# Kernel tuning notes

Measured on AMD Instinct MI355X. Metric: run time of the kernel, lower is better.

## Reference

```python
import jax, jax.numpy as jnp
import numpy as np

D_MODEL = 1024
NUM_HEADS = 16
D_K = D_MODEL // NUM_HEADS
THETA = 10000.0


def setup_inputs() -> dict:
    key = jax.random.key(0)
    ks = jax.random.split(key, 5)
    B, S = 2, 2048
    sigma = np.sqrt(2.0 / (D_MODEL + D_MODEL))
    x = jax.random.normal(ks[0], (B, S, D_MODEL), dtype=jnp.float32)
    Wq = jax.random.normal(ks[1], (D_MODEL, D_MODEL), dtype=jnp.float32) * sigma
    Wk = jax.random.normal(ks[2], (D_MODEL, D_MODEL), dtype=jnp.float32) * sigma
    Wv = jax.random.normal(ks[3], (D_MODEL, D_MODEL), dtype=jnp.float32) * sigma
    Wo = jax.random.normal(ks[4], (D_MODEL, D_MODEL), dtype=jnp.float32) * sigma
    return {"x": x, "Wq": Wq, "Wk": Wk, "Wv": Wv, "Wo": Wo}


def _rope(x, cos, sin):
    # x: [B, H, S, D_K]; cos/sin: [S, D_K//2] broadcast to [1, 1, S, D_K//2]
    x1 = x[..., ::2]
    x2 = x[..., 1::2]
    even = x1 * cos - x2 * sin
    odd = x1 * sin + x2 * cos
    return jnp.stack((even, odd), axis=-1).reshape(x.shape)


def reference(x, Wq, Wk, Wv, Wo):
    B, S, _ = x.shape
    # projections: weight is (out, in), applied as einsum('oi,...i->...o')
    q = jnp.einsum('oi,bsi->bso', Wq, x).reshape(B, S, NUM_HEADS, D_K).transpose(0, 2, 1, 3)
    k = jnp.einsum('oi,bsi->bso', Wk, x).reshape(B, S, NUM_HEADS, D_K).transpose(0, 2, 1, 3)
    v = jnp.einsum('oi,bsi->bso', Wv, x).reshape(B, S, NUM_HEADS, D_K).transpose(0, 2, 1, 3)
    # RoPE tables (token_positions = arange(S))
    inv_freq = 1.0 / (THETA ** (jnp.arange(0, D_K, 2, dtype=jnp.float32) / D_K))
    t = jnp.arange(S, dtype=jnp.float32)
    freqs = t[:, None] * inv_freq[None, :]          # [S, D_K/2]
    cos = jnp.cos(freqs)[None, None]                # [1,1,S,D_K/2]
    sin = jnp.sin(freqs)[None, None]
    q = _rope(q, cos, sin)
    k = _rope(k, cos, sin)
    # causal attention, full materialized scores (faithful to source)
    scores = jnp.einsum('bhid,bhjd->bhij', q, k) / np.sqrt(D_K).astype(np.float32)
    causal = jnp.tril(jnp.ones((S, S), dtype=bool))
    scores = jnp.where(causal, scores, -jnp.inf)
    attn = jax.nn.softmax(scores, axis=-1)
    out = jnp.einsum('bhij,bhjd->bhid', attn, v)    # [B,H,S,D_K]
    out = out.transpose(0, 2, 1, 3).reshape(B, S, D_MODEL)
    return jnp.einsum('oi,bsi->bso', Wo, out)
```

## Files before the change

### kernel.cpp

```cpp
#include <hip/hip_runtime.h>

#define D_MODEL 1024
#define NUM_HEADS 16
#define SEQ 2048
#define BATCH 2

typedef __attribute__((ext_vector_type(8))) short bf16x8;
typedef __attribute__((ext_vector_type(4))) float f32x4;

__device__ __forceinline__ float bf2f(unsigned short u) {
    return __uint_as_float(((unsigned int)u) << 16);
}
__device__ __forceinline__ unsigned short f2bf(float f) {
    unsigned int u = __float_as_uint(f);
    return (unsigned short)((u + 0x7FFFu + ((u >> 16) & 1u)) >> 16);
}
__device__ __forceinline__ ushort4 pack4(float4 v) {
    return make_ushort4(f2bf(v.x), f2bf(v.y), f2bf(v.z), f2bf(v.w));
}

__device__ __forceinline__ void gload_lds16(const unsigned short* g, unsigned short* l) {
    __builtin_amdgcn_global_load_lds(
        (const __attribute__((address_space(1))) unsigned int*)g,
        (__attribute__((address_space(3))) unsigned int*)l,
        16, 0, 0);
}

__device__ __forceinline__ bf16x8 lds_read_swz(const unsigned short (*tile)[64], int row, int chunk) {
    const char* p = reinterpret_cast<const char*>(tile);
    return *reinterpret_cast<const bf16x8*>(p + row * 128 + (((chunk ^ (row & 7))) << 4));
}

__device__ __forceinline__ bf16x8 lds_read_swz32(const unsigned short (*tile)[32], int row, int chunk) {
    const char* p = reinterpret_cast<const char*>(tile);
    return *reinterpret_cast<const bf16x8*>(p + row * 64 + (((chunk ^ (row & 3))) << 4));
}

__device__ __forceinline__ bf16x8 lds_read_swz128(const unsigned short (*tile)[128], int row, int chunk) {
    const char* p = reinterpret_cast<const char*>(tile);
    return *reinterpret_cast<const bf16x8*>(p + row * 256 + (((chunk ^ (row & 15))) << 4));
}

__global__ __launch_bounds__(256) void conv_kernel(
    const float* __restrict__ src, unsigned short* __restrict__ dst, int n4)
{
    int i = blockIdx.x * 256 + threadIdx.x;
    if (i < n4) {
        float4 v = reinterpret_cast<const float4*>(src)[i];
        reinterpret_cast<ushort4*>(dst)[i] = pack4(v);
    }
}

__global__ __launch_bounds__(256) void conv4_kernel(
    const float* __restrict__ x, const float* __restrict__ Wq,
    const float* __restrict__ Wk, const float* __restrict__ Wv,
    unsigned short* __restrict__ xb, unsigned short* __restrict__ w3bf,
    float2* __restrict__ tab)
{
    int i = blockIdx.x * 256 + threadIdx.x;
    if (i < 1835008) {
        const float* src;
        unsigned short* dst;
        int off;
        if (i < 1048576) {
            src = x; dst = xb; off = i;
        } else {
            int j = i - 1048576;
            int which = j >> 18;
            off = j & 0x3FFFF;
            src = (which == 0) ? Wq : (which == 1) ? Wk : Wv;
            dst = w3bf + ((size_t)which << 20);
        }
        float4 v = reinterpret_cast<const float4*>(src)[off];
        reinterpret_cast<ushort4*>(dst)[off] = pack4(v);
    } else {
        int idx = i - 1835008;
        int s = idx >> 5, d2 = idx & 31;
        float inv = powf(10000.0f, -(float)d2 / 32.0f);
        float sn, cs;
        sincosf((float)s * inv, &sn, &cs);
        tab[idx] = make_float2(cs, sn);
    }
}

__global__ __launch_bounds__(256) void qkv_mfma_kernel(
    const unsigned short* __restrict__ xb,
    const unsigned short* __restrict__ w3,
    const float2* __restrict__ tab,
    unsigned short* __restrict__ qb, unsigned short* __restrict__ kb,
    unsigned short* __restrict__ vt)
{
    const int lin = blockIdx.x;
    const int b = lin & 7;
    const int t = lin >> 3;
    const int which = t % 3;
    const int y = t / 3;
    const unsigned short* __restrict__ W = w3 + (size_t)which * 1048576;
    const int m0 = y * 128;
    const int n0g = b * 128;

    __shared__ __align__(16) unsigned short As[2][128][32];
    __shared__ __align__(16) unsigned short Bs[2][128][32];

    const int tid = threadIdx.x;
    const int w = tid >> 6;
    const int lane = tid & 63;
    const int quad = lane >> 4;
    const int c15 = lane & 15;
    const int qm = w >> 1, qn = w & 1;
    const int srow4 = lane >> 2;
    const int sch4 = lane & 3;

    auto stage = [&](int k0, int buf) {
#pragma unroll
        for (int i = 0; i < 2; i++) {
            const int row = i * 64 + w * 16 + srow4;
            const int ch = sch4 ^ (row & 3);
            gload_lds16(xb + (size_t)(m0 + row) * 1024 + k0 + ch * 8,
                        &As[buf][i * 64 + w * 16][0]);
            gload_lds16(W + (size_t)(n0g + row) * 1024 + k0 + ch * 8,
                        &Bs[buf][i * 64 + w * 16][0]);
        }
    };

    f32x4 acc[4][4];
#pragma unroll
    for (int mi = 0; mi < 4; mi++)
#pragma unroll
        for (int ni = 0; ni < 4; ni++) acc[mi][ni] = (f32x4){0.f, 0.f, 0.f, 0.f};

    stage(0, 0);
    for (int k0 = 0; k0 < 1024; k0 += 32) {
        const int cb = (k0 >> 5) & 1;
        __syncthreads();
        if (k0 < 992) stage(k0 + 32, cb ^ 1);

        bf16x8 af[4], bfr[4];
#pragma unroll
        for (int mi = 0; mi < 4; mi++)
            af[mi] = lds_read_swz32(As[cb], qm * 64 + mi * 16 + c15, quad);
#pragma unroll
        for (int ni = 0; ni < 4; ni++)
            bfr[ni] = lds_read_swz32(Bs[cb], qn * 64 + ni * 16 + c15, quad);
#pragma unroll
        for (int mi = 0; mi < 4; mi++)
#pragma unroll
            for (int ni = 0; ni < 4; ni++)
                acc[mi][ni] = __builtin_amdgcn_mfma_f32_16x16x32_bf16(af[mi], bfr[ni], acc[mi][ni], 0, 0, 0);
    }

    __syncthreads();
    unsigned short* stg = &As[0][0][0] + w * (16 * 72);
    const int hq = b * 2 + qn;
    unsigned short* outp = (which == 0) ? qb : kb;
    const int odd = c15 & 1;

#pragma unroll
    for (int mi = 0; mi < 4; mi++) {
#pragma unroll
        for (int r = 0; r < 4; r++) {
            int m = m0 + qm * 64 + mi * 16 + quad * 4 + r;
            int s = m & (SEQ - 1);
            const float2* trow = tab + (s << 5);
#pragma unroll
            for (int ni = 0; ni < 4; ni++) {
                float val = acc[mi][ni][r];
                float res;
                if (which < 2) {
                    float part = __shfl_xor(val, 1);
                    float2 cs = trow[(ni * 16 + c15) >> 1];
                    res = odd ? (part * cs.y + val * cs.x) : (val * cs.x - part * cs.y);
                } else {
                    res = val;
                }
                stg[(quad * 4 + r) * 72 + ni * 16 + c15] = f2bf(res);
            }
        }
        if (which < 2) {
            int row = lane >> 2;
            int ch = lane & 3;
            int m = m0 + qm * 64 + mi * 16 + row;
            int s = m & (SEQ - 1);
            int bb = m >> 11;
            size_t ob = (((size_t)bb * NUM_HEADS + hq) * SEQ + s) * 64 + ch * 16;
            uint4 v0 = *reinterpret_cast<const uint4*>(&stg[row * 72 + ch * 16]);
            uint4 v1 = *reinterpret_cast<const uint4*>(&stg[row * 72 + ch * 16 + 8]);
            *reinterpret_cast<uint4*>(&outp[ob]) = v0;
            *reinterpret_cast<uint4*>(&outp[ob + 8]) = v1;
        } else {
            int mbase = m0 + qm * 64 + mi * 16;
            int bb = mbase >> 11;
            int s_base = mbase & (SEQ - 1);
            unsigned short tmp[16];
#pragma unroll
            for (int sl = 0; sl < 16; sl++) tmp[sl] = stg[sl * 72 + lane];
            size_t ob = (((size_t)bb * NUM_HEADS + hq) * 64 + lane) * SEQ + s_base;
            *reinterpret_cast<uint4*>(&vt[ob])     = *reinterpret_cast<uint4*>(&tmp[0]);
            *reinterpret_cast<uint4*>(&vt[ob + 8]) = *reinterpret_cast<uint4*>(&tmp[8]);
        }
    }
}

__global__ __launch_bounds__(256) void attn_kernel(
    const unsigned short* __restrict__ qb, const unsigned short* __restrict__ kb,
    const unsigned short* __restrict__ vt, unsigned short* __restrict__ ab)
{
    const int xpair = blockIdx.x;
    const int bh = blockIdx.y;
    const int b = bh >> 4, h = bh & 15;
    const size_t base = (size_t)bh * SEQ * 64;
    const size_t vbase = (size_t)bh * 64 * SEQ;
    const int tid = threadIdx.x;
    const int w = tid >> 6;
    const int lane = tid & 63;
    const int quad = lane >> 4;
    const int c15 = lane & 15;
    const int srow8 = lane >> 3;
    const int sch = lane & 7;
    const int srow16 = lane >> 4;
    const int sch16 = lane & 15;
    const float C = 0.125f;

    __shared__ __align__(16) unsigned short Ks[2][128][64];
    __shared__ __align__(16) unsigned short Vs[2][64][128];
    __shared__ __align__(16) unsigned short Pl[64][72];

    auto stage = [&](int sj, int buf) {
        const int j0s = sj * 128;
#pragma unroll
        for (int i = 0; i < 4; i++) {
            const int krow = w * 32 + i * 8 + srow8;
            const int kch = sch ^ (krow & 7);
            gload_lds16(kb + base + (size_t)(j0s + krow) * 64 + kch * 8,
                        &Ks[buf][w * 32 + i * 8][0]);
            const int vrow = w * 16 + i * 4 + srow16;
            const int vch = sch16 ^ (vrow & 15);
            gload_lds16(vt + vbase + (size_t)vrow * SEQ + j0s + vch * 8,
                        &Vs[buf][w * 16 + i * 4][0]);
        }
    };

    for (int pass = 0; pass < 2; pass++) {
        const int it = pass ? xpair : (31 - xpair);
        const int i0 = it * 64;
        const int nj = (it >> 1) + 1;

        const int qrow = i0 + w * 16 + c15;
        bf16x8 qf0 = *reinterpret_cast<const bf16x8*>(&qb[base + (size_t)qrow * 64 + quad * 8]);
        bf16x8 qf1 = *reinterpret_cast<const bf16x8*>(&qb[base + (size_t)qrow * 64 + 32 + quad * 8]);

        float m_st = -1e30f, l_st = 0.f;
        f32x4 Oc[4];
#pragma unroll
        for (int t = 0; t < 4; t++) Oc[t] = (f32x4){0.f, 0.f, 0.f, 0.f};

        __syncthreads();
        stage(0, 0);

        for (int sj = 0; sj < nj; sj++) {
            const int cb = sj & 1;

            __syncthreads();
            if (sj < nj - 1) stage(sj + 1, cb ^ 1);

#pragma unroll
            for (int hf = 0; hf < 2; hf++) {
                const int j0 = sj * 128 + hf * 64;
                if (j0 > i0) continue;

                bf16x8 kc0[4], kc1[4];
#pragma unroll
                for (int t = 0; t < 4; t++) {
                    kc0[t] = lds_read_swz(Ks[cb], hf * 64 + t * 16 + c15, quad);
                    kc1[t] = lds_read_swz(Ks[cb], hf * 64 + t * 16 + c15, 4 + quad);
                }

                f32x4 sc[4];
#pragma unroll
                for (int t = 0; t < 4; t++) sc[t] = (f32x4){0.f, 0.f, 0.f, 0.f};
                __builtin_amdgcn_s_setprio(1);
#pragma unroll
                for (int t = 0; t < 4; t++) {
                    sc[t] = __builtin_amdgcn_mfma_f32_16x16x32_bf16(kc0[t], qf0, sc[t], 0, 0, 0);
                    sc[t] = __builtin_amdgcn_mfma_f32_16x16x32_bf16(kc1[t], qf1, sc[t], 0, 0, 0);
                }
                __builtin_amdgcn_s_setprio(0);

                bf16x8 vv0[4], vv1[4];
#pragma unroll
                for (int t = 0; t < 4; t++) {
                    vv0[t] = lds_read_swz128(Vs[cb], t * 16 + c15, hf * 8 + quad);
                    vv1[t] = lds_read_swz128(Vs[cb], t * 16 + c15, hf * 8 + 4 + quad);
                }

                if (j0 == i0) {
                    const int gi = i0 + w * 16 + c15;
#pragma unroll
                    for (int t = 0; t < 4; t++) {
#pragma unroll
                        for (int r = 0; r < 4; r++) {
                            int gj = j0 + t * 16 + quad * 4 + r;
                            if (gj > gi) sc[t][r] = -1e30f;
                        }
                    }
                }

                float x0 = fmaxf(fmaxf(sc[0][0], sc[0][1]), fmaxf(sc[0][2], sc[0][3]));
                float x1 = fmaxf(fmaxf(sc[1][0], sc[1][1]), fmaxf(sc[1][2], sc[1][3]));
                float x2 = fmaxf(fmaxf(sc[2][0], sc[2][1]), fmaxf(sc[2][2], sc[2][3]));
                float x3 = fmaxf(fmaxf(sc[3][0], sc[3][1]), fmaxf(sc[3][2], sc[3][3]));
                float tm = fmaxf(fmaxf(x0, x1), fmaxf(x2, x3));
                tm = fmaxf(tm, __shfl_xor(tm, 16));
                tm = fmaxf(tm, __shfl_xor(tm, 32));

                if (!__all(tm <= m_st + 64.0f)) {
                    float mnew = fmaxf(m_st, tm);
                    float alpha = __expf((m_st - mnew) * C);
                    l_st *= alpha;
#pragma unroll
                    for (int t = 0; t < 4; t++)
#pragma unroll
                        for (int r = 0; r < 4; r++) Oc[t][r] *= alpha;
                    m_st = mnew;
                }

                const float mC = m_st * C;
                float p[4][4];
#pragma unroll
                for (int t = 0; t < 4; t++)
#pragma unroll
                    for (int r = 0; r < 4; r++)
                        p[t][r] = __expf(__builtin_fmaf(sc[t][r], C, -mC));

                float s0 = (p[0][0] + p[0][1]) + (p[0][2] + p[0][3]);
                float s1 = (p[1][0] + p[1][1]) + (p[1][2] + p[1][3]);
                float s2 = (p[2][0] + p[2][1]) + (p[2][2] + p[2][3]);
                float s3 = (p[3][0] + p[3][1]) + (p[3][2] + p[3][3]);
                l_st += (s0 + s1) + (s2 + s3);

#pragma unroll
                for (int t = 0; t < 4; t++) {
#pragma unroll
                    for (int hh = 0; hh < 2; hh++) {
                        unsigned int pk = (unsigned int)f2bf(p[t][2 * hh])
                                        | ((unsigned int)f2bf(p[t][2 * hh + 1]) << 16);
                        *reinterpret_cast<unsigned int*>(
                            &Pl[w * 16 + c15][t * 16 + quad * 4 + 2 * hh]) = pk;
                    }
                }

                bf16x8 ap0 = *reinterpret_cast<const bf16x8*>(&Pl[w * 16 + c15][quad * 8]);
                bf16x8 ap1 = *reinterpret_cast<const bf16x8*>(&Pl[w * 16 + c15][32 + quad * 8]);
                __builtin_amdgcn_s_setprio(1);
#pragma unroll
                for (int t = 0; t < 4; t++) {
                    Oc[t] = __builtin_amdgcn_mfma_f32_16x16x32_bf16(vv0[t], ap0, Oc[t], 0, 0, 0);
                    Oc[t] = __builtin_amdgcn_mfma_f32_16x16x32_bf16(vv1[t], ap1, Oc[t], 0, 0, 0);
                }
                __builtin_amdgcn_s_setprio(0);
            }
        }

        l_st += __shfl_xor(l_st, 16);
        l_st += __shfl_xor(l_st, 32);
        float inv = 1.0f / l_st;
#pragma unroll
        for (int t = 0; t < 4; t++) {
#pragma unroll
            for (int hh = 0; hh < 2; hh++) {
                unsigned int pk = (unsigned int)f2bf(Oc[t][2 * hh] * inv)
                                | ((unsigned int)f2bf(Oc[t][2 * hh + 1] * inv) << 16);
                *reinterpret_cast<unsigned int*>(
                    &Pl[w * 16 + c15][t * 16 + quad * 4 + 2 * hh]) = pk;
            }
        }
        {
            int row = lane >> 2;
            int ch = lane & 3;
            int gi = i0 + w * 16 + row;
            size_t ob = ((size_t)b * SEQ + gi) * 1024 + h * 64 + ch * 16;
            uint4 v0 = *reinterpret_cast<const uint4*>(&Pl[w * 16 + row][ch * 16]);
            uint4 v1 = *reinterpret_cast<const uint4*>(&Pl[w * 16 + row][ch * 16 + 8]);
            *reinterpret_cast<uint4*>(&ab[ob]) = v0;
            *reinterpret_cast<uint4*>(&ab[ob + 8]) = v1;
        }
    }
}

__global__ __launch_bounds__(256) void out_mfma_kernel(
    const unsigned short* __restrict__ A, const unsigned short* __restrict__ Wob,
    float* __restrict__ out)
{
    const int lin = blockIdx.x;
    const int b = lin & 7;
    const int y = lin >> 3;
    const int m0 = y * 64;
    const int n0g = b * 128;

    __shared__ __align__(16) unsigned short As[2][64][32];
    __shared__ __align__(16) unsigned short Bs[2][128][32];

    const int tid = threadIdx.x;
    const int w = tid >> 6;
    const int lane = tid & 63;
    const int quad = lane >> 4;
    const int c15 = lane & 15;
    const int qm = w >> 1, qn = w & 1;
    const int srow4 = lane >> 2;
    const int sch4 = lane & 3;

    auto stage = [&](int k0, int buf) {
        {
            const int row = w * 16 + srow4;
            const int ch = sch4 ^ (row & 3);
            gload_lds16(A + (size_t)(m0 + row) * 1024 + k0 + ch * 8,
                        &As[buf][w * 16][0]);
        }
#pragma unroll
        for (int i = 0; i < 2; i++) {
            const int row = i * 64 + w * 16 + srow4;
            const int ch = sch4 ^ (row & 3);
            gload_lds16(Wob + (size_t)(n0g + row) * 1024 + k0 + ch * 8,
                        &Bs[buf][i * 64 + w * 16][0]);
        }
    };

    f32x4 acc[2][4];
#pragma unroll
    for (int mi = 0; mi < 2; mi++)
#pragma unroll
        for (int ni = 0; ni < 4; ni++) acc[mi][ni] = (f32x4){0.f, 0.f, 0.f, 0.f};

    stage(0, 0);
    for (int k0 = 0; k0 < 1024; k0 += 32) {
        const int cb = (k0 >> 5) & 1;
        __syncthreads();
        if (k0 < 992) stage(k0 + 32, cb ^ 1);

        bf16x8 af[2], bfr[4];
#pragma unroll
        for (int mi = 0; mi < 2; mi++)
            af[mi] = lds_read_swz32(As[cb], qm * 32 + mi * 16 + c15, quad);
#pragma unroll
        for (int ni = 0; ni < 4; ni++)
            bfr[ni] = lds_read_swz32(Bs[cb], qn * 64 + ni * 16 + c15, quad);
#pragma unroll
        for (int mi = 0; mi < 2; mi++)
#pragma unroll
            for (int ni = 0; ni < 4; ni++)
                acc[mi][ni] = __builtin_amdgcn_mfma_f32_16x16x32_bf16(af[mi], bfr[ni], acc[mi][ni], 0, 0, 0);
    }

#pragma unroll
    for (int mi = 0; mi < 2; mi++) {
#pragma unroll
        for (int r = 0; r < 4; r++) {
            int m = m0 + qm * 32 + mi * 16 + quad * 4 + r;
#pragma unroll
            for (int ni = 0; ni < 4; ni++) {
                int n = n0g + qn * 64 + ni * 16 + c15;
                out[(size_t)m * 1024 + n] = acc[mi][ni][r];
            }
        }
    }
}

extern "C" void kernel_launch(void* const* d_in, const int* in_sizes, int n_in,
                              void* d_out, int out_size, void* d_ws, size_t ws_size,
                              hipStream_t stream)
{
    const float* x  = (const float*)d_in[0];
    const float* Wq = (const float*)d_in[1];
    const float* Wk = (const float*)d_in[2];
    const float* Wv = (const float*)d_in[3];
    const float* Wo = (const float*)d_in[4];
    float* out = (float*)d_out;

    const size_t QKV_ELEMS = (size_t)BATCH * SEQ * D_MODEL;

    unsigned short* qb = (unsigned short*)d_ws;
    unsigned short* kb = qb + QKV_ELEMS;
    unsigned short* vt = kb + QKV_ELEMS;
    unsigned short* ab = vt + QKV_ELEMS;
    unsigned short* w3bf = ab;
    unsigned short* wobf = qb;
    unsigned short* xbuf = (unsigned short*)d_out;
    float2* tab = (float2*)((char*)d_out + 8 * 1024 * 1024);

    conv4_kernel<<<dim3(7424), 256, 0, stream>>>(x, Wq, Wk, Wv, xbuf, w3bf, tab);
    qkv_mfma_kernel<<<dim3(768), 256, 0, stream>>>(xbuf, w3bf, tab, qb, kb, vt);
    attn_kernel<<<dim3(16, 32), 256, 0, stream>>>(qb, kb, vt, ab);
    conv_kernel<<<dim3(1024), 256, 0, stream>>>(Wo, wobf, 262144);
    out_mfma_kernel<<<dim3(512), 256, 0, stream>>>(ab, wobf, out);
}
```

Measured before the change: 202.3 us.

## Split attention KV tile across two wave groups with merged softmax states

Doubles the attention block to 512 threads so two groups of four waves each process one 64-column half of every 128-key tile in parallel, then merges their online-softmax states (max, sum, partial O) through shared memory at the end. The P matrix is now packed with v_cvt_pk_bf16_f32 and redistributed via cross-lane shuffles instead of a round trip through LDS. Staging work per thread is halved. This aims for more in-flight waves and shorter per-wave serial chains, at the cost of extra synchronisation and an end-of-tile reduction that reuses the K/V LDS buffers.

```diff
diff --git a/kernel.cpp b/kernel.cpp
--- a/kernel.cpp
+++ b/kernel.cpp
@@ -201,7 +201,7 @@
     }
 }
 
-__global__ __launch_bounds__(256) void attn_kernel(
+__global__ __launch_bounds__(512, 4) void attn_kernel(
     const unsigned short* __restrict__ qb, const unsigned short* __restrict__ kb,
     const unsigned short* __restrict__ vt, unsigned short* __restrict__ ab)
 {
@@ -212,6 +212,8 @@
     const size_t vbase = (size_t)bh * 64 * SEQ;
     const int tid = threadIdx.x;
     const int w = tid >> 6;
+    const int grp = w >> 2;
+    const int wa = w & 3;
     const int lane = tid & 63;
     const int quad = lane >> 4;
     const int c15 = lane & 15;
@@ -223,20 +225,22 @@
 
     __shared__ __align__(16) unsigned short Ks[2][128][64];
     __shared__ __align__(16) unsigned short Vs[2][64][128];
-    __shared__ __align__(16) unsigned short Pl[64][72];
+    float* exch = (float*)&Ks[0][0][0];
+    float2* ml  = (float2*)((char*)&Ks[0][0][0] + 17152);
+    unsigned short* ost = &Vs[0][0][0];
 
     auto stage = [&](int sj, int buf) {
         const int j0s = sj * 128;
 #pragma unroll
-        for (int i = 0; i < 4; i++) {
-            const int krow = w * 32 + i * 8 + srow8;
+        for (int i = 0; i < 2; i++) {
+            const int krow = w * 16 + i * 8 + srow8;
             const int kch = sch ^ (krow & 7);
             gload_lds16(kb + base + (size_t)(j0s + krow) * 64 + kch * 8,
-                        &Ks[buf][w * 32 + i * 8][0]);
-            const int vrow = w * 16 + i * 4 + srow16;
+                        &Ks[buf][w * 16 + i * 8][0]);
+            const int vrow = w * 8 + i * 4 + srow16;
             const int vch = sch16 ^ (vrow & 15);
             gload_lds16(vt + vbase + (size_t)vrow * SEQ + j0s + vch * 8,
-                        &Vs[buf][w * 16 + i * 4][0]);
+                        &Vs[buf][w * 8 + i * 4][0]);
         }
     };
 
@@ -245,7 +249,7 @@
         const int i0 = it * 64;
         const int nj = (it >> 1) + 1;
 
-        const int qrow = i0 + w * 16 + c15;
+        const int qrow = i0 + wa * 16 + c15;
         bf16x8 qf0 = *reinterpret_cast<const bf16x8*>(&qb[base + (size_t)qrow * 64 + quad * 8]);
         bf16x8 qf1 = *reinterpret_cast<const bf16x8*>(&qb[base + (size_t)qrow * 64 + 32 + quad * 8]);
 
@@ -259,20 +263,16 @@
 
         for (int sj = 0; sj < nj; sj++) {
             const int cb = sj & 1;
-
             __syncthreads();
             if (sj < nj - 1) stage(sj + 1, cb ^ 1);
 
-#pragma unroll
-            for (int hf = 0; hf < 2; hf++) {
-                const int j0 = sj * 128 + hf * 64;
-                if (j0 > i0) continue;
-
+            const int j0 = sj * 128 + grp * 64;
+            if (j0 <= i0) {
                 bf16x8 kc0[4], kc1[4];
 #pragma unroll
                 for (int t = 0; t < 4; t++) {
-                    kc0[t] = lds_read_swz(Ks[cb], hf * 64 + t * 16 + c15, quad);
-                    kc1[t] = lds_read_swz(Ks[cb], hf * 64 + t * 16 + c15, 4 + quad);
+                    kc0[t] = lds_read_swz(Ks[cb], grp * 64 + t * 16 + c15, quad);
+                    kc1[t] = lds_read_swz(Ks[cb], grp * 64 + t * 16 + c15, 4 + quad);
                 }
 
                 f32x4 sc[4];
@@ -289,12 +289,12 @@
                 bf16x8 vv0[4], vv1[4];
 #pragma unroll
                 for (int t = 0; t < 4; t++) {
-                    vv0[t] = lds_read_swz128(Vs[cb], t * 16 + c15, hf * 8 + quad);
-                    vv1[t] = lds_read_swz128(Vs[cb], t * 16 + c15, hf * 8 + 4 + quad);
+                    vv0[t] = lds_read_swz128(Vs[cb], t * 16 + c15, grp * 8 + quad);
+                    vv1[t] = lds_read_swz128(Vs[cb], t * 16 + c15, grp * 8 + 4 + quad);
                 }
 
                 if (j0 == i0) {
-                    const int gi = i0 + w * 16 + c15;
+                    const int gi = i0 + wa * 16 + c15;
 #pragma unroll
                     for (int t = 0; t < 4; t++) {
 #pragma unroll
@@ -338,19 +338,30 @@
                 float s3 = (p[3][0] + p[3][1]) + (p[3][2] + p[3][3]);
                 l_st += (s0 + s1) + (s2 + s3);
 
-#pragma unroll
-                for (int t = 0; t < 4; t++) {
-#pragma unroll
-                    for (int hh = 0; hh < 2; hh++) {
-                        unsigned int pk = (unsigned int)f2bf(p[t][2 * hh])
-                                        | ((unsigned int)f2bf(p[t][2 * hh + 1]) << 16);
-                        *reinterpret_cast<unsigned int*>(
-                            &Pl[w * 16 + c15][t * 16 + quad * 4 + 2 * hh]) = pk;
-                    }
-                }
-
-                bf16x8 ap0 = *reinterpret_cast<const bf16x8*>(&Pl[w * 16 + c15][quad * 8]);
-                bf16x8 ap1 = *reinterpret_cast<const bf16x8*>(&Pl[w * 16 + c15][32 + quad * 8]);
+                unsigned int pk[4][2];
+#pragma unroll
+                for (int t = 0; t < 4; t++)
+#pragma unroll
+                    for (int hh = 0; hh < 2; hh++)
+                        asm("v_cvt_pk_bf16_f32 %0, %1, %2"
+                            : "=v"(pk[t][hh]) : "v"(p[t][2 * hh]), "v"(p[t][2 * hh + 1]));
+
+                unsigned int w0[4], w1[4];
+#pragma unroll
+                for (int e = 0; e < 4; e++) {
+                    int sl = c15 + 16 * ((2 * quad + (e >> 1)) & 3);
+                    unsigned int a0 = (unsigned int)__shfl((int)pk[0][e & 1], sl);
+                    unsigned int b0 = (unsigned int)__shfl((int)pk[1][e & 1], sl);
+                    w0[e] = (quad >> 1) ? b0 : a0;
+                    unsigned int a1 = (unsigned int)__shfl((int)pk[2][e & 1], sl);
+                    unsigned int b1 = (unsigned int)__shfl((int)pk[3][e & 1], sl);
+                    w1[e] = (quad >> 1) ? b1 : a1;
+                }
+                uint4 u0 = make_uint4(w0[0], w0[1], w0[2], w0[3]);
+                uint4 u1 = make_uint4(w1[0], w1[1], w1[2], w1[3]);
+                bf16x8 ap0 = *reinterpret_cast<bf16x8*>(&u0);
+                bf16x8 ap1 = *reinterpret_cast<bf16x8*>(&u1);
+
                 __builtin_amdgcn_s_setprio(1);
 #pragma unroll
                 for (int t = 0; t < 4; t++) {
@@ -361,28 +372,50 @@
             }
         }
 
-        l_st += __shfl_xor(l_st, 16);
-        l_st += __shfl_xor(l_st, 32);
-        float inv = 1.0f / l_st;
-#pragma unroll
-        for (int t = 0; t < 4; t++) {
-#pragma unroll
-            for (int hh = 0; hh < 2; hh++) {
-                unsigned int pk = (unsigned int)f2bf(Oc[t][2 * hh] * inv)
-                                | ((unsigned int)f2bf(Oc[t][2 * hh + 1] * inv) << 16);
-                *reinterpret_cast<unsigned int*>(
-                    &Pl[w * 16 + c15][t * 16 + quad * 4 + 2 * hh]) = pk;
+        __syncthreads();
+        float l_row = l_st;
+        l_row += __shfl_xor(l_row, 16);
+        l_row += __shfl_xor(l_row, 32);
+        const int q = wa * 16 + c15;
+
+        if (grp == 1) {
+#pragma unroll
+            for (int t = 0; t < 4; t++)
+#pragma unroll
+                for (int r = 0; r < 4; r++)
+                    exch[q * 65 + t * 16 + quad * 4 + r] = Oc[t][r];
+            if (quad == 0) ml[q] = make_float2(m_st, l_row);
+        }
+        __syncthreads();
+        if (grp == 0) {
+            float2 mlB = ml[q];
+            float m = fmaxf(m_st, mlB.x);
+            float aA = __expf((m_st - m) * C);
+            float aB = __expf((mlB.x - m) * C);
+            float inv = 1.0f / (l_row * aA + mlB.y * aB);
+#pragma unroll
+            for (int t = 0; t < 4; t++) {
+#pragma unroll
+                for (int hh = 0; hh < 2; hh++) {
+                    float o0 = (Oc[t][2 * hh] * aA
+                                + exch[q * 65 + t * 16 + quad * 4 + 2 * hh] * aB) * inv;
+                    float o1 = (Oc[t][2 * hh + 1] * aA
+                                + exch[q * 65 + t * 16 + quad * 4 + 2 * hh + 1] * aB) * inv;
+                    unsigned int pko = (unsigned int)f2bf(o0) | ((unsigned int)f2bf(o1) << 16);
+                    *reinterpret_cast<unsigned int*>(
+                        &ost[q * 72 + t * 16 + quad * 4 + 2 * hh]) = pko;
+                }
             }
-        }
-        {
-            int row = lane >> 2;
-            int ch = lane & 3;
-            int gi = i0 + w * 16 + row;
-            size_t ob = ((size_t)b * SEQ + gi) * 1024 + h * 64 + ch * 16;
-            uint4 v0 = *reinterpret_cast<const uint4*>(&Pl[w * 16 + row][ch * 16]);
-            uint4 v1 = *reinterpret_cast<const uint4*>(&Pl[w * 16 + row][ch * 16 + 8]);
-            *reinterpret_cast<uint4*>(&ab[ob]) = v0;
-            *reinterpret_cast<uint4*>(&ab[ob + 8]) = v1;
+            {
+                int row = lane >> 2;
+                int ch = lane & 3;
+                int gi = i0 + wa * 16 + row;
+                size_t ob = ((size_t)b * SEQ + gi) * 1024 + h * 64 + ch * 16;
+                uint4 v0 = *reinterpret_cast<const uint4*>(&ost[(wa * 16 + row) * 72 + ch * 16]);
+                uint4 v1 = *reinterpret_cast<const uint4*>(&ost[(wa * 16 + row) * 72 + ch * 16 + 8]);
+                *reinterpret_cast<uint4*>(&ab[ob]) = v0;
+                *reinterpret_cast<uint4*>(&ab[ob + 8]) = v1;
+            }
         }
     }
 }
@@ -489,7 +522,7 @@
 
     conv4_kernel<<<dim3(7424), 256, 0, stream>>>(x, Wq, Wk, Wv, xbuf, w3bf, tab);
     qkv_mfma_kernel<<<dim3(768), 256, 0, stream>>>(xbuf, w3bf, tab, qb, kb, vt);
-    attn_kernel<<<dim3(16, 32), 256, 0, stream>>>(qb, kb, vt, ab);
+    attn_kernel<<<dim3(16, 32), 512, 0, stream>>>(qb, kb, vt, ab);
     conv_kernel<<<dim3(1024), 256, 0, stream>>>(Wo, wobf, 262144);
     out_mfma_kernel<<<dim3(512), 256, 0, stream>>>(ab, wobf, out);
 }
```

Measured after the change: 199.8 us. No clear change (-1.3%).
